# Kernel tuning notes

Hardware: AMD Instinct MI355X
Metric: run time of the kernel (lower is better)

## Reference

```python
import jax, jax.numpy as jnp
import numpy as np

NUM_HEADS = 16

def setup_inputs() -> dict:
    key = jax.random.key(0)
    k1, k2, k3 = jax.random.split(key, 3)
    B, T, C = 2, 2048, 1024
    x = jax.random.normal(k1, (B, T, C), dtype=jnp.float32)
    w_qkv = jax.random.normal(k2, (C, 3 * C), dtype=jnp.float32) * (1.0 / np.sqrt(C))
    b_qkv = jnp.zeros((3 * C,), dtype=jnp.float32)
    w_out = jax.random.normal(k3, (C, C), dtype=jnp.float32) * (1.0 / np.sqrt(C))
    b_out = jnp.zeros((C,), dtype=jnp.float32)
    return {"x": x, "w_qkv": w_qkv, "b_qkv": b_qkv, "w_out": w_out, "b_out": b_out}

def reference(x, w_qkv, b_qkv, w_out, b_out):
    B, T, C = x.shape
    H = NUM_HEADS
    D = C // H
    qkv = x @ w_qkv + b_qkv                      # [B,T,3C]
    q, k, v = jnp.split(qkv, 3, axis=-1)
    # [B,T,C] -> [B,H,T,D]
    q = q.reshape(B, T, H, D).transpose(0, 2, 1, 3)
    k = k.reshape(B, T, H, D).transpose(0, 2, 1, 3)
    v = v.reshape(B, T, H, D).transpose(0, 2, 1, 3)
    scale = 1.0 / jnp.sqrt(jnp.asarray(D, dtype=x.dtype))
    scores = jnp.einsum('bhqd,bhkd->bhqk', q, k) * scale  # [B,H,T,T]
    causal = jnp.tril(jnp.ones((T, T), dtype=bool))
    scores = jnp.where(causal, scores, jnp.asarray(-jnp.inf, dtype=scores.dtype))
    attn = jax.nn.softmax(scores, axis=-1)
    out = jnp.einsum('bhqk,bhkd->bhqd', attn, v)          # [B,H,T,D]
    out = out.transpose(0, 2, 1, 3).reshape(B, T, C)
    return out @ w_out + b_out
```

## Files before the change

### kernel.cpp

```cpp
#include <hip/hip_runtime.h>
#include <hip/hip_bf16.h>

#define MHSA_B 2
#define MHSA_T 2048
#define MHSA_C 1024
#define MHSA_H 16
#define MHSA_D 64

typedef __attribute__((ext_vector_type(8))) short bf16x8_t;
typedef __attribute__((ext_vector_type(4))) float f32x4_t;

__device__ __forceinline__ unsigned short f2bf(float f) {
    unsigned int u = __float_as_uint(f);
    u = u + 0x7FFFu + ((u >> 16) & 1u);
    return (unsigned short)(u >> 16);
}

__device__ __forceinline__ void gload_lds16(const void* g, void* l) {
    __builtin_amdgcn_global_load_lds(
        (const __attribute__((address_space(1))) void*)g,
        (__attribute__((address_space(3))) void*)l, 16, 0, 0);
}

__device__ __forceinline__ float rowred_max(float t) {
    t = fmaxf(t, __shfl_xor(t, 1));
    t = fmaxf(t, __shfl_xor(t, 2));
    t = fmaxf(t, __shfl_xor(t, 4));
    t = fmaxf(t, __shfl_xor(t, 8));
    return t;
}
__device__ __forceinline__ float rowred_sum(float t) {
    t += __shfl_xor(t, 1);
    t += __shfl_xor(t, 2);
    t += __shfl_xor(t, 4);
    t += __shfl_xor(t, 8);
    return t;
}

__global__ __launch_bounds__(256)
void f32_to_bf16_kernel(const float* __restrict__ in,
                        unsigned short* __restrict__ out, int n4) {
    int i = blockIdx.x * blockDim.x + threadIdx.x;
    const int stride = gridDim.x * blockDim.x;
    for (; i < n4; i += stride) {
        float4 v = *(const float4*)&in[(size_t)i * 4];
        ushort4 u;
        u.x = f2bf(v.x); u.y = f2bf(v.y); u.z = f2bf(v.z); u.w = f2bf(v.w);
        *(ushort4*)&out[(size_t)i * 4] = u;
    }
}

__global__ __launch_bounds__(256)
void transpose_to_bf16_kernel(const float* __restrict__ W,
                              unsigned short* __restrict__ WT,
                              int R, int Ncols) {
    __shared__ float tile[32][33];
    const int c0 = blockIdx.x * 32;
    const int r0 = blockIdx.y * 32;
    const int tx = threadIdx.x & 31;
    const int ty = threadIdx.x >> 5;
#pragma unroll
    for (int i = 0; i < 32; i += 8)
        tile[ty + i][tx] = W[(size_t)(r0 + ty + i) * Ncols + c0 + tx];
    __syncthreads();
#pragma unroll
    for (int i = 0; i < 32; i += 8)
        WT[(size_t)(c0 + ty + i) * R + r0 + tx] = f2bf(tile[tx][ty + i]);
}

template <int MODE>
__global__ __launch_bounds__(256)
void gemm_bf16_mfma(const unsigned short* __restrict__ A,
                    const unsigned short* __restrict__ Bt,
                    const float* __restrict__ bias,
                    void* __restrict__ Cout,
                    unsigned short* __restrict__ vtb,
                    int M, int N, int K) {
    __shared__ unsigned short As[128 * 32];
    __shared__ unsigned short Bs[128 * 32];

    const int tid  = threadIdx.x;
    const int lane = tid & 63;
    const int w    = tid >> 6;
    const int bm   = blockIdx.y * 128;
    const int bn   = blockIdx.x * 128;
    const int wr   = (w >> 1) * 64;
    const int wc   = (w & 1) * 64;

    f32x4_t acc[4][4];
#pragma unroll
    for (int m = 0; m < 4; ++m)
#pragma unroll
        for (int n = 0; n < 4; ++n) acc[m][n] = (f32x4_t){0.f, 0.f, 0.f, 0.f};

    const int rS = lane >> 2;
    const int kS = (lane & 3) * 8;

    for (int k0 = 0; k0 < K; k0 += 32) {
        __syncthreads();
#pragma unroll
        for (int c = 0; c < 2; ++c) {
            const int row = c * 64 + w * 16 + rS;
            gload_lds16(&A[(size_t)(bm + row) * K + k0 + kS],
                        &As[c * 2048 + w * 512]);
            gload_lds16(&Bt[(size_t)(bn + row) * K + k0 + kS],
                        &Bs[c * 2048 + w * 512]);
        }
        __syncthreads();

        bf16x8_t a[4], b[4];
#pragma unroll
        for (int m = 0; m < 4; ++m)
            a[m] = *(const bf16x8_t*)&As[(wr + m * 16 + (lane & 15)) * 32 + (lane >> 4) * 8];
#pragma unroll
        for (int n = 0; n < 4; ++n)
            b[n] = *(const bf16x8_t*)&Bs[(wc + n * 16 + (lane & 15)) * 32 + (lane >> 4) * 8];
#pragma unroll
        for (int m = 0; m < 4; ++m)
#pragma unroll
            for (int n = 0; n < 4; ++n)
                acc[m][n] = __builtin_amdgcn_mfma_f32_16x16x32_bf16(a[m], b[n], acc[m][n], 0, 0, 0);
    }

    const int cq = lane >> 4;
    const int cr = lane & 15;
#pragma unroll
    for (int n = 0; n < 4; ++n) {
        const int col = bn + wc + n * 16 + cr;
        const float bv = bias[col];
        const int rowb = bm + wr + cq * 4;
#pragma unroll
        for (int m = 0; m < 4; ++m) {
            if (MODE == 2 && col >= 2 * MHSA_C) {
                const int vcol = col - 2 * MHSA_C;
                const int h = vcol >> 6;
                const int d = vcol & 63;
                const int tg = rowb + m * 16;
                const int bb = tg >> 11;
                const int tt = tg & (MHSA_T - 1);
                ushort4 u;
                u.x = f2bf(acc[m][n][0] + bv);
                u.y = f2bf(acc[m][n][1] + bv);
                u.z = f2bf(acc[m][n][2] + bv);
                u.w = f2bf(acc[m][n][3] + bv);
                *(ushort4*)&vtb[(size_t)((bb * 16 + h) * 64 + d) * MHSA_T + tt] = u;
            } else {
#pragma unroll
                for (int r = 0; r < 4; ++r) {
                    const int row = rowb + m * 16 + r;
                    const float val = acc[m][n][r] + bv;
                    if (MODE == 0)
                        ((float*)Cout)[(size_t)row * N + col] = val;
                    else
                        ((unsigned short*)Cout)[(size_t)row * N + col] = f2bf(val);
                }
            }
        }
    }
}

__global__ __launch_bounds__(64, 2)
void attn_mfma_kernel(const unsigned short* __restrict__ qkvb,
                      const unsigned short* __restrict__ vtb,
                      unsigned short* __restrict__ attb) {
    constexpr int T = MHSA_T, C = MHSA_C;
    constexpr int C3 = 3 * C;
    constexpr int LS = 72;

    __shared__ unsigned short Ps[32 * LS];

    const int l = threadIdx.x;
    const int c = l & 15;
    const int g = l >> 4;
    const int idx = blockIdx.x;
    const int bh = idx & 31;
    const int h = bh & 15;
    const int b = bh >> 4;
    const int qt = 63 - (idx >> 5);
    const int q0 = qt * 32;
    const size_t rowbase = (size_t)(b * T) * C3;

    bf16x8_t qf[2][2];
    const unsigned short* Qg = qkvb + rowbase + (size_t)q0 * C3 + h * 64;
#pragma unroll
    for (int m = 0; m < 2; ++m)
#pragma unroll
        for (int ks = 0; ks < 2; ++ks)
            qf[m][ks] = *(const bf16x8_t*)(Qg + (size_t)(m * 16 + c) * C3 + ks * 32 + g * 8);

    f32x4_t acc_o[2][4];
#pragma unroll
    for (int m = 0; m < 2; ++m)
#pragma unroll
        for (int dn = 0; dn < 4; ++dn) acc_o[m][dn] = (f32x4_t){0.f, 0.f, 0.f, 0.f};
    float mrun[2][4], lrun[2][4];
#pragma unroll
    for (int m = 0; m < 2; ++m)
#pragma unroll
        for (int j = 0; j < 4; ++j) { mrun[m][j] = -1e30f; lrun[m][j] = 0.f; }

    const unsigned short* Kg = qkvb + rowbase + C + h * 64;
    const unsigned short* Vg = vtb + (size_t)(bh * 64) * T;

    for (int k0 = 0; k0 <= q0 + 31; k0 += 64) {
        bf16x8_t kf[4][2];
#pragma unroll
        for (int n = 0; n < 4; ++n)
#pragma unroll
            for (int ks = 0; ks < 2; ++ks)
                kf[n][ks] = *(const bf16x8_t*)(Kg + (size_t)(k0 + n * 16 + c) * C3 + ks * 32 + g * 8);

        f32x4_t sA[2][4];
#pragma unroll
        for (int m = 0; m < 2; ++m)
#pragma unroll
            for (int n = 0; n < 4; ++n) sA[m][n] = (f32x4_t){0.f, 0.f, 0.f, 0.f};
#pragma unroll
        for (int ks = 0; ks < 2; ++ks)
#pragma unroll
            for (int m = 0; m < 2; ++m)
#pragma unroll
                for (int n = 0; n < 4; ++n)
                    sA[m][n] = __builtin_amdgcn_mfma_f32_16x16x32_bf16(qf[m][ks], kf[n][ks], sA[m][n], 0, 0, 0);

        bf16x8_t vf[4][2];
#pragma unroll
        for (int dn = 0; dn < 4; ++dn)
#pragma unroll
            for (int ks = 0; ks < 2; ++ks)
                vf[dn][ks] = *(const bf16x8_t*)(Vg + (size_t)(dn * 16 + c) * T + k0 + ks * 32 + g * 8);

        const bool diag = (k0 + 64 > q0);
#pragma unroll
        for (int m = 0; m < 2; ++m)
#pragma unroll
            for (int n = 0; n < 4; ++n)
#pragma unroll
                for (int j = 0; j < 4; ++j) {
                    float sv = sA[m][n][j] * 0.125f;
                    if (diag) {
                        const int col = k0 + n * 16 + c;
                        const int row = q0 + m * 16 + g * 4 + j;
                        sv = (col <= row) ? sv : -1e30f;
                    }
                    sA[m][n][j] = sv;
                }

#pragma unroll
        for (int m = 0; m < 2; ++m)
#pragma unroll
            for (int j = 0; j < 4; ++j) {
                float t = fmaxf(fmaxf(sA[m][0][j], sA[m][1][j]),
                                fmaxf(sA[m][2][j], sA[m][3][j]));
                t = rowred_max(t);
                const float mn = fmaxf(mrun[m][j], t);
                const float scl = __expf(mrun[m][j] - mn);
                mrun[m][j] = mn;
#pragma unroll
                for (int dn = 0; dn < 4; ++dn) acc_o[m][dn][j] *= scl;
                float ps = 0.f;
#pragma unroll
                for (int n = 0; n < 4; ++n) {
                    const float p = __expf(sA[m][n][j] - mn);
                    Ps[(m * 16 + g * 4 + j) * LS + n * 16 + c] = f2bf(p);
                    ps += p;
                }
                ps = rowred_sum(ps);
                lrun[m][j] = lrun[m][j] * scl + ps;
            }
        __syncthreads();

#pragma unroll
        for (int ks = 0; ks < 2; ++ks) {
            bf16x8_t pf[2];
#pragma unroll
            for (int m = 0; m < 2; ++m)
                pf[m] = *(const bf16x8_t*)&Ps[(m * 16 + c) * LS + ks * 32 + g * 8];
#pragma unroll
            for (int m = 0; m < 2; ++m)
#pragma unroll
                for (int dn = 0; dn < 4; ++dn)
                    acc_o[m][dn] = __builtin_amdgcn_mfma_f32_16x16x32_bf16(pf[m], vf[dn][ks], acc_o[m][dn], 0, 0, 0);
        }
    }

    unsigned short* Og = attb + (size_t)(b * T + q0) * C + h * 64;
#pragma unroll
    for (int m = 0; m < 2; ++m)
#pragma unroll
        for (int j = 0; j < 4; ++j) {
            const float inv = 1.f / lrun[m][j];
#pragma unroll
            for (int dn = 0; dn < 4; ++dn)
                Og[(size_t)(m * 16 + g * 4 + j) * C + dn * 16 + c] =
                    f2bf(acc_o[m][dn][j] * inv);
        }
}

extern "C" void kernel_launch(void* const* d_in, const int* in_sizes, int n_in,
                              void* d_out, int out_size, void* d_ws, size_t ws_size,
                              hipStream_t stream) {
    const float* x     = (const float*)d_in[0];
    const float* w_qkv = (const float*)d_in[1];
    const float* b_qkv = (const float*)d_in[2];
    const float* w_out = (const float*)d_in[3];
    const float* b_out = (const float*)d_in[4];
    float* out = (float*)d_out;

    constexpr int BT = MHSA_B * MHSA_T;
    constexpr int C  = MHSA_C;
    constexpr int C3 = 3 * C;

    unsigned short* qkvb  = (unsigned short*)d_ws;
    unsigned short* vtb   = qkvb + (size_t)BT * C3;
    unsigned short* xb    = vtb + (size_t)2048 * 2048;
    unsigned short* attb  = xb + (size_t)BT * C;
    unsigned short* wqkvT = attb + (size_t)BT * C;
    unsigned short* woutT = wqkvT + (size_t)C3 * C;

    f32_to_bf16_kernel<<<2048, 256, 0, stream>>>(x, xb, BT * C / 4);
    transpose_to_bf16_kernel<<<dim3(C3 / 32, C / 32), 256, 0, stream>>>(
        w_qkv, wqkvT, C, C3);
    transpose_to_bf16_kernel<<<dim3(C / 32, C / 32), 256, 0, stream>>>(
        w_out, woutT, C, C);

    gemm_bf16_mfma<2><<<dim3(C3 / 128, BT / 128), 256, 0, stream>>>(
        xb, wqkvT, b_qkv, qkvb, vtb, BT, C3, C);

    attn_mfma_kernel<<<dim3(2048), dim3(64), 0, stream>>>(qkvb, vtb, attb);

    gemm_bf16_mfma<0><<<dim3(C / 128, BT / 128), 256, 0, stream>>>(
        attb, woutT, b_out, out, nullptr, BT, C, C);
}
```

Measured before the change: 260.5 us.

## Stage K and V tiles through swizzled LDS via direct global-to-LDS loads

The attention kernel now copies each 64x64 K and V tile into shared memory with global_load_lds, using an XOR swizzle on the 16-byte chunks, and reads the MFMA operands back from LDS. Before, each lane gathered K and V fragments directly from global memory with strided row loads. The aim is coalesced global traffic and conflict-free LDS reads. In exchange it adds two barriers per key tile and 16 KB of LDS per block, and there is no double buffering, so load latency is no longer overlapped with compute.

```diff
diff --git a/kernel.cpp b/kernel.cpp
--- a/kernel.cpp
+++ b/kernel.cpp
@@ -167,6 +167,8 @@
     constexpr int C3 = 3 * C;
     constexpr int LS = 72;
 
+    __shared__ unsigned short Ks[64 * 64];
+    __shared__ unsigned short Vs[64 * 64];
     __shared__ unsigned short Ps[32 * LS];
 
     const int l = threadIdx.x;
@@ -180,6 +182,10 @@
     const int q0 = qt * 32;
     const size_t rowbase = (size_t)(b * T) * C3;
 
+    const int sr = l >> 3;
+    const int sc = l & 7;
+    const int schunk = (sc ^ sr) * 8;
+
     bf16x8_t qf[2][2];
     const unsigned short* Qg = qkvb + rowbase + (size_t)q0 * C3 + h * 64;
 #pragma unroll
@@ -203,12 +209,14 @@
     const unsigned short* Vg = vtb + (size_t)(bh * 64) * T;
 
     for (int k0 = 0; k0 <= q0 + 31; k0 += 64) {
-        bf16x8_t kf[4][2];
-#pragma unroll
-        for (int n = 0; n < 4; ++n)
-#pragma unroll
-            for (int ks = 0; ks < 2; ++ks)
-                kf[n][ks] = *(const bf16x8_t*)(Kg + (size_t)(k0 + n * 16 + c) * C3 + ks * 32 + g * 8);
+        __syncthreads();
+#pragma unroll
+        for (int i = 0; i < 8; ++i) {
+            const int r = i * 8 + sr;
+            gload_lds16(Kg + (size_t)(k0 + r) * C3 + schunk, &Ks[i * 512]);
+            gload_lds16(Vg + (size_t)r * T + k0 + schunk, &Vs[i * 512]);
+        }
+        __syncthreads();
 
         f32x4_t sA[2][4];
 #pragma unroll
@@ -216,19 +224,19 @@
 #pragma unroll
             for (int n = 0; n < 4; ++n) sA[m][n] = (f32x4_t){0.f, 0.f, 0.f, 0.f};
 #pragma unroll
-        for (int ks = 0; ks < 2; ++ks)
+        for (int ks = 0; ks < 2; ++ks) {
+            bf16x8_t kf[4];
+#pragma unroll
+            for (int n = 0; n < 4; ++n) {
+                const int row = n * 16 + c;
+                kf[n] = *(const bf16x8_t*)&Ks[row * 64 + (((ks * 4 + g) ^ (row & 7)) * 8)];
+            }
 #pragma unroll
             for (int m = 0; m < 2; ++m)
 #pragma unroll
                 for (int n = 0; n < 4; ++n)
-                    sA[m][n] = __builtin_amdgcn_mfma_f32_16x16x32_bf16(qf[m][ks], kf[n][ks], sA[m][n], 0, 0, 0);
-
-        bf16x8_t vf[4][2];
-#pragma unroll
-        for (int dn = 0; dn < 4; ++dn)
-#pragma unroll
-            for (int ks = 0; ks < 2; ++ks)
-                vf[dn][ks] = *(const bf16x8_t*)(Vg + (size_t)(dn * 16 + c) * T + k0 + ks * 32 + g * 8);
+                    sA[m][n] = __builtin_amdgcn_mfma_f32_16x16x32_bf16(qf[m][ks], kf[n], sA[m][n], 0, 0, 0);
+        }
 
         const bool diag = (k0 + 64 > q0);
 #pragma unroll
@@ -272,15 +280,20 @@
 
 #pragma unroll
         for (int ks = 0; ks < 2; ++ks) {
-            bf16x8_t pf[2];
+            bf16x8_t pf[2], vf[4];
 #pragma unroll
             for (int m = 0; m < 2; ++m)
                 pf[m] = *(const bf16x8_t*)&Ps[(m * 16 + c) * LS + ks * 32 + g * 8];
 #pragma unroll
+            for (int dn = 0; dn < 4; ++dn) {
+                const int row = dn * 16 + c;
+                vf[dn] = *(const bf16x8_t*)&Vs[row * 64 + (((ks * 4 + g) ^ (row & 7)) * 8)];
+            }
+#pragma unroll
             for (int m = 0; m < 2; ++m)
 #pragma unroll
                 for (int dn = 0; dn < 4; ++dn)
-                    acc_o[m][dn] = __builtin_amdgcn_mfma_f32_16x16x32_bf16(pf[m], vf[dn][ks], acc_o[m][dn], 0, 0, 0);
+                    acc_o[m][dn] = __builtin_amdgcn_mfma_f32_16x16x32_bf16(pf[m], vf[dn], acc_o[m][dn], 0, 0, 0);
         }
     }
 
```

Result: slower. 268.0 us (+2.9%).
